# Performance work log

Measured on AMD Instinct MI355X. Metric: run time of the kernel, lower is better.

Reference implementation:

```python
import math
import jax, jax.numpy as jnp
import numpy as np

N, L, D, H = 2, 2048, 1024, 16
DK = D // H  # 64


def setup_inputs() -> dict:
    key = jax.random.key(0)
    k1, k2, k3, k4, k5 = jax.random.split(key, 5)
    scale = 1.0 / math.sqrt(D)
    return {
        "values": jax.random.normal(k1, (N, L, D), dtype=jnp.float32),
        "keys": jax.random.normal(k2, (N, L, D), dtype=jnp.float32),
        "queries": jax.random.normal(k3, (N, L, D), dtype=jnp.float32),
        "fc_out_w": jax.random.normal(k4, (D, D), dtype=jnp.float32) * scale,
        "fc_out_b": jax.random.normal(k5, (D,), dtype=jnp.float32) * scale,
    }


def reference(values, keys, queries, fc_out_w, fc_out_b):
    n, q_len, _ = queries.shape
    k_len = keys.shape[1]
    v = values.reshape(n, k_len, H, DK)
    k = keys.reshape(n, k_len, H, DK)
    q = queries.reshape(n, q_len, H, DK)
    # NOTE: the original module never applies its per-head Linear layers (dead code),
    # and scales logits AFTER the QK einsum.
    energy = jnp.einsum('nqhd,nkhd->nhqk', q, k)  # [N,H,q,k]
    p_attn = jax.nn.softmax(energy / math.sqrt(DK), axis=3)
    attn = jnp.einsum('nhqk,nkhd->nqhd', p_attn, v).reshape(n, q_len, H * DK)
    # fc_out: torch Linear -> x @ W.T + b
    return attn @ fc_out_w.T + fc_out_b
```

## Files before the change

### kernel.cpp

```cpp
#include <hip/hip_runtime.h>
#include <hip/hip_bf16.h>

#define NBATCH 2
#define SEQ    2048
#define DMODEL 1024
#define NHEAD  16
#define DHEAD  64
#define NHTOT  (NBATCH*NHEAD)

typedef __attribute__((ext_vector_type(8))) short          short8;
typedef __attribute__((ext_vector_type(4))) float          f32x4;
typedef __attribute__((ext_vector_type(4))) unsigned short ushort4v;

__device__ __forceinline__ unsigned short f2bf(float x) {
  union { __hip_bfloat16 b; unsigned short u; } c;
  c.b = __float2bfloat16(x);
  return c.u;
}

__device__ __forceinline__ void gl_lds16(const unsigned short* g, unsigned short* l) {
  __builtin_amdgcn_global_load_lds(
      (const __attribute__((address_space(1))) void*)g,
      (__attribute__((address_space(3))) void*)l, 16, 0, 0);
}

__global__ __launch_bounds__(256) void cvt_qk(const float* __restrict__ q,
                                              const float* __restrict__ k,
                                              unsigned short* __restrict__ qb,
                                              unsigned short* __restrict__ kb) {
  const float QSCALE = 0.125f * 1.44269504088896340736f;
  int e = (blockIdx.x * 256 + threadIdx.x) * 4;
  int n = e >> 21;
  int r = e & ((1 << 21) - 1);
  int l = r >> 10;
  int c = r & 1023;
  int h = c >> 6;
  int d = c & 63;
  size_t dst = ((size_t)(n * NHEAD + h) * SEQ + l) * DHEAD + d;
  float4 qv = *reinterpret_cast<const float4*>(q + e);
  float4 kv = *reinterpret_cast<const float4*>(k + e);
  ushort4v qo, ko;
  qo.x = f2bf(qv.x * QSCALE); qo.y = f2bf(qv.y * QSCALE);
  qo.z = f2bf(qv.z * QSCALE); qo.w = f2bf(qv.w * QSCALE);
  ko.x = f2bf(kv.x); ko.y = f2bf(kv.y); ko.z = f2bf(kv.z); ko.w = f2bf(kv.w);
  *reinterpret_cast<ushort4v*>(qb + dst) = qo;
  *reinterpret_cast<ushort4v*>(kb + dst) = ko;
}

__global__ __launch_bounds__(256) void vtrans(const float* __restrict__ v,
                                              unsigned short* __restrict__ vt) {
  __shared__ unsigned short t[64][66];
  int bid = blockIdx.x;
  int nh = bid >> 5;
  int lt = bid & 31;
  int n = nh >> 4, h = nh & 15;
  int lbase = lt * 64;
  #pragma unroll
  for (int j = 0; j < 16; ++j) {
    int e = j * 256 + threadIdx.x;
    int l = e >> 6, d = e & 63;
    float x = v[((size_t)n * SEQ + lbase + l) * DMODEL + h * DHEAD + d];
    t[l][d] = f2bf(x);
  }
  __syncthreads();
  #pragma unroll
  for (int j = 0; j < 16; ++j) {
    int e = j * 256 + threadIdx.x;
    int d = e >> 6, l = e & 63;
    vt[((size_t)nh * DHEAD + d) * SEQ + lbase + l] = t[l][d];
  }
}

__global__ __launch_bounds__(256) void cvt_w(const float* __restrict__ w,
                                             unsigned short* __restrict__ wb) {
  int e = (blockIdx.x * 256 + threadIdx.x) * 4;
  float4 wv = *reinterpret_cast<const float4*>(w + e);
  ushort4v wo;
  wo.x = f2bf(wv.x); wo.y = f2bf(wv.y); wo.z = f2bf(wv.z); wo.w = f2bf(wv.w);
  *reinterpret_cast<ushort4v*>(wb + e) = wo;
}

__global__ __launch_bounds__(256) void attn_fwd(const unsigned short* __restrict__ Qb,
                                                const unsigned short* __restrict__ Kb,
                                                const unsigned short* __restrict__ Vt,
                                                unsigned short* __restrict__ Ab) {
  __shared__ __align__(16) unsigned short kbuf[2][64 * 64];
  __shared__ __align__(16) unsigned short vbuf[2][64 * 64];
  __shared__ __align__(16) unsigned short pbuf[4][16][72];

  const int bid = blockIdx.x;
  const int nh = bid >> 5;
  const int qt = bid & 31;
  const int tid = threadIdx.x;
  const int wave = tid >> 6;
  const int lane = tid & 63;
  const int l15 = lane & 15, l4 = lane >> 4;

  const unsigned short* Kb_nh = Kb + (size_t)nh * SEQ * DHEAD;
  const unsigned short* Vt_nh = Vt + (size_t)nh * DHEAD * SEQ;

  const unsigned short* Qrow =
      Qb + ((size_t)nh * SEQ + qt * 64 + wave * 16 + l15) * DHEAD + l4 * 8;
  short8 bq0 = *reinterpret_cast<const short8*>(Qrow);
  short8 bq1 = *reinterpret_cast<const short8*>(Qrow + 32);

  float m_run = -3.0e38f, l_run = 0.f;
  f32x4 acc[4];
  #pragma unroll
  for (int d = 0; d < 4; ++d) acc[d] = (f32x4){0.f, 0.f, 0.f, 0.f};

  auto stage = [&](int buf, int kk) {
    #pragma unroll
    for (int j = 0; j < 2; ++j) {
      int c = j * 256 + tid;
      int row = c >> 3, cs = c & 7;
      int cg = cs ^ (row & 7);
      int cb = j * 256 + (tid & 192);
      gl_lds16(Kb_nh + (size_t)(kk + row) * DHEAD + cg * 8, &kbuf[buf][cb * 8]);
      gl_lds16(Vt_nh + (size_t)row * SEQ + kk + cg * 8, &vbuf[buf][cb * 8]);
    }
  };

  stage(0, 0);
  __syncthreads();

  const int NT = SEQ / 64;
  for (int it = 0; it < NT; ++it) {
    int cur = it & 1;
    if (it + 1 < NT) stage(cur ^ 1, (it + 1) * 64);

    const unsigned short* kb = kbuf[cur];
    const unsigned short* vb = vbuf[cur];

    f32x4 s[4];
    #pragma unroll
    for (int t = 0; t < 4; ++t) {
      int row = t * 16 + l15;
      int sw = row & 7;
      short8 ak0 = *reinterpret_cast<const short8*>(kb + row * 64 + ((l4 ^ sw) * 8));
      short8 ak1 = *reinterpret_cast<const short8*>(kb + row * 64 + (((l4 + 4) ^ sw) * 8));
      f32x4 z = (f32x4){0.f, 0.f, 0.f, 0.f};
      z = __builtin_amdgcn_mfma_f32_16x16x32_bf16(ak0, bq0, z, 0, 0, 0);
      z = __builtin_amdgcn_mfma_f32_16x16x32_bf16(ak1, bq1, z, 0, 0, 0);
      s[t] = z;
    }

    float mx = s[0][0];
    #pragma unroll
    for (int t = 0; t < 4; ++t)
      #pragma unroll
      for (int r = 0; r < 4; ++r) mx = fmaxf(mx, s[t][r]);
    mx = fmaxf(mx, __shfl_xor(mx, 16));
    mx = fmaxf(mx, __shfl_xor(mx, 32));
    float mnew = fmaxf(m_run, mx);
    float corr = exp2f(m_run - mnew);
    m_run = mnew;
    float sum = 0.f;
    #pragma unroll
    for (int t = 0; t < 4; ++t)
      #pragma unroll
      for (int r = 0; r < 4; ++r) {
        float p = exp2f(s[t][r] - mnew);
        s[t][r] = p;
        sum += p;
      }
    sum += __shfl_xor(sum, 16);
    sum += __shfl_xor(sum, 32);
    l_run = l_run * corr + sum;

    #pragma unroll
    for (int r = 0; r < 4; ++r) {
      float cb_ = __shfl(corr, l4 * 4 + r);
      #pragma unroll
      for (int dd = 0; dd < 4; ++dd) acc[dd][r] *= cb_;
    }

    #pragma unroll
    for (int t = 0; t < 4; ++t) {
      ushort4v pk;
      pk.x = f2bf(s[t][0]); pk.y = f2bf(s[t][1]);
      pk.z = f2bf(s[t][2]); pk.w = f2bf(s[t][3]);
      *reinterpret_cast<ushort4v*>(&pbuf[wave][l15][t * 16 + l4 * 4]) = pk;
    }
    asm volatile("s_waitcnt lgkmcnt(0)" ::: "memory");
    __builtin_amdgcn_sched_barrier(0);
    short8 pa0 = *reinterpret_cast<const short8*>(&pbuf[wave][l15][l4 * 8]);
    short8 pa1 = *reinterpret_cast<const short8*>(&pbuf[wave][l15][32 + l4 * 8]);

    #pragma unroll
    for (int dd = 0; dd < 4; ++dd) {
      int row = dd * 16 + l15;
      int sw = row & 7;
      short8 bv0 = *reinterpret_cast<const short8*>(vb + row * 64 + ((l4 ^ sw) * 8));
      short8 bv1 = *reinterpret_cast<const short8*>(vb + row * 64 + (((l4 + 4) ^ sw) * 8));
      acc[dd] = __builtin_amdgcn_mfma_f32_16x16x32_bf16(pa0, bv0, acc[dd], 0, 0, 0);
      acc[dd] = __builtin_amdgcn_mfma_f32_16x16x32_bf16(pa1, bv1, acc[dd], 0, 0, 0);
    }
    __syncthreads();
  }

  int n = nh >> 4, hd = nh & 15;
  #pragma unroll
  for (int r = 0; r < 4; ++r) {
    float lf = __shfl(l_run, l4 * 4 + r);
    float inv = 1.0f / lf;
    size_t ob = ((size_t)n * SEQ + qt * 64 + wave * 16 + l4 * 4 + r) * DMODEL +
                hd * DHEAD;
    #pragma unroll
    for (int dd = 0; dd < 4; ++dd)
      Ab[ob + dd * 16 + l15] = f2bf(acc[dd][r] * inv);
  }
}

__global__ __launch_bounds__(256) void fc_gemm(const unsigned short* __restrict__ Ab,
                                               const unsigned short* __restrict__ Wb,
                                               const float* __restrict__ bias,
                                               float* __restrict__ out) {
  __shared__ __align__(16) unsigned short At[2][64 * 32];
  __shared__ __align__(16) unsigned short Bt[2][64 * 32];
  const int bid = blockIdx.x;
  const int bm = bid >> 4;
  const int bn = bid & 15;
  const int tid = threadIdx.x;
  const int wave = tid >> 6, lane = tid & 63;
  const int wr = wave >> 1, wc = wave & 1;
  const int l15 = lane & 15, l4 = lane >> 4;

  f32x4 acc[2][2];
  #pragma unroll
  for (int i = 0; i < 2; ++i)
    #pragma unroll
    for (int j = 0; j < 2; ++j) acc[i][j] = (f32x4){0.f, 0.f, 0.f, 0.f};

  auto stage = [&](int buf, int k0) {
    int row = tid >> 2, cs = tid & 3;
    int cb = tid & 192;
    gl_lds16(Ab + (size_t)(bm * 64 + row) * DMODEL + k0 + cs * 8, &At[buf][cb * 8]);
    gl_lds16(Wb + (size_t)(bn * 64 + row) * DMODEL + k0 + cs * 8, &Bt[buf][cb * 8]);
  };

  stage(0, 0);
  __syncthreads();

  const int NT = DMODEL / 32;
  for (int it = 0; it < NT; ++it) {
    int cur = it & 1;
    if (it + 1 < NT) stage(cur ^ 1, (it + 1) * 32);

    short8 a0 = *reinterpret_cast<const short8*>(&At[cur][(wr * 32 + l15) * 32 + l4 * 8]);
    short8 a1 = *reinterpret_cast<const short8*>(&At[cur][(wr * 32 + 16 + l15) * 32 + l4 * 8]);
    short8 b0 = *reinterpret_cast<const short8*>(&Bt[cur][(wc * 32 + l15) * 32 + l4 * 8]);
    short8 b1 = *reinterpret_cast<const short8*>(&Bt[cur][(wc * 32 + 16 + l15) * 32 + l4 * 8]);
    acc[0][0] = __builtin_amdgcn_mfma_f32_16x16x32_bf16(a0, b0, acc[0][0], 0, 0, 0);
    acc[0][1] = __builtin_amdgcn_mfma_f32_16x16x32_bf16(a0, b1, acc[0][1], 0, 0, 0);
    acc[1][0] = __builtin_amdgcn_mfma_f32_16x16x32_bf16(a1, b0, acc[1][0], 0, 0, 0);
    acc[1][1] = __builtin_amdgcn_mfma_f32_16x16x32_bf16(a1, b1, acc[1][1], 0, 0, 0);
    __syncthreads();
  }

  #pragma unroll
  for (int m = 0; m < 2; ++m)
    #pragma unroll
    for (int nn = 0; nn < 2; ++nn) {
      int col = bn * 64 + wc * 32 + nn * 16 + l15;
      float bv = bias[col];
      #pragma unroll
      for (int r = 0; r < 4; ++r) {
        int row = bm * 64 + wr * 32 + m * 16 + l4 * 4 + r;
        out[(size_t)row * DMODEL + col] = acc[m][nn][r] + bv;
      }
    }
}

extern "C" void kernel_launch(void* const* d_in, const int* in_sizes, int n_in,
                              void* d_out, int out_size, void* d_ws, size_t ws_size,
                              hipStream_t stream) {
  const float* values  = (const float*)d_in[0];
  const float* keys    = (const float*)d_in[1];
  const float* queries = (const float*)d_in[2];
  const float* fc_w    = (const float*)d_in[3];
  const float* fc_b    = (const float*)d_in[4];
  float* out = (float*)d_out;

  char* ws = (char*)d_ws;
  const size_t QKV_BYTES = (size_t)NHTOT * SEQ * DHEAD * 2;
  unsigned short* Qb = (unsigned short*)(ws);
  unsigned short* Kb = (unsigned short*)(ws + QKV_BYTES);
  unsigned short* Vt = (unsigned short*)(ws + 2 * QKV_BYTES);
  unsigned short* Wb = (unsigned short*)(ws + 3 * QKV_BYTES);
  unsigned short* Ab = (unsigned short*)(ws + 3 * QKV_BYTES + (size_t)DMODEL * DMODEL * 2);

  cvt_qk<<<4096, 256, 0, stream>>>(queries, keys, Qb, Kb);
  vtrans<<<1024, 256, 0, stream>>>(values, Vt);
  cvt_w<<<1024, 256, 0, stream>>>(fc_w, Wb);
  attn_fwd<<<NHTOT * (SEQ / 64), 256, 0, stream>>>(Qb, Kb, Vt, Ab);
  fc_gemm<<<(NBATCH * SEQ / 64) * (DMODEL / 64), 256, 0, stream>>>(Ab, Wb, fc_b, out);
}
```

Measured before the change: 220.1 us.

## Restructure attention with 32x32 MFMA, register P permute, lazy rescale, and bigger GEMM tiles

```diff
diff --git a/kernel.cpp b/kernel.cpp
--- a/kernel.cpp
+++ b/kernel.cpp
@@ -8,14 +8,21 @@
 #define DHEAD  64
 #define NHTOT  (NBATCH*NHEAD)
 
-typedef __attribute__((ext_vector_type(8))) short          short8;
-typedef __attribute__((ext_vector_type(4))) float          f32x4;
-typedef __attribute__((ext_vector_type(4))) unsigned short ushort4v;
+typedef __attribute__((ext_vector_type(8)))  short          short8;
+typedef __attribute__((ext_vector_type(4)))  float          f32x4;
+typedef __attribute__((ext_vector_type(16))) float          f32x16;
+typedef __attribute__((ext_vector_type(4)))  unsigned short ushort4v;
 
 __device__ __forceinline__ unsigned short f2bf(float x) {
   union { __hip_bfloat16 b; unsigned short u; } c;
   c.b = __float2bfloat16(x);
   return c.u;
+}
+
+__device__ __forceinline__ unsigned int cvt_pk_bf16(float lo, float hi) {
+  unsigned int r;
+  asm("v_cvt_pk_bf16_f32 %0, %1, %2" : "=v"(r) : "v"(lo), "v"(hi));
+  return r;
 }
 
 __device__ __forceinline__ void gl_lds16(const unsigned short* g, unsigned short* l) {
@@ -80,45 +87,49 @@
   *reinterpret_cast<ushort4v*>(wb + e) = wo;
 }
 
-__global__ __launch_bounds__(256) void attn_fwd(const unsigned short* __restrict__ Qb,
-                                                const unsigned short* __restrict__ Kb,
-                                                const unsigned short* __restrict__ Vt,
-                                                unsigned short* __restrict__ Ab) {
+__global__ __launch_bounds__(512, 2) void attn_fwd(const unsigned short* __restrict__ Qb,
+                                                   const unsigned short* __restrict__ Kb,
+                                                   const unsigned short* __restrict__ Vt,
+                                                   unsigned short* __restrict__ Ab) {
   __shared__ __align__(16) unsigned short kbuf[2][64 * 64];
   __shared__ __align__(16) unsigned short vbuf[2][64 * 64];
-  __shared__ __align__(16) unsigned short pbuf[4][16][72];
+  __shared__ __align__(16) unsigned short obuf[4][32][72];
 
   const int bid = blockIdx.x;
-  const int nh = bid >> 5;
-  const int qt = bid & 31;
-  const int tid = threadIdx.x;
+  const int nh = (bid & 7) * 4 + (bid >> 6);
+  const int qt = (bid >> 3) & 7;
+  const int tid  = threadIdx.x;
   const int wave = tid >> 6;
   const int lane = tid & 63;
-  const int l15 = lane & 15, l4 = lane >> 4;
+  const int l31  = lane & 31;
+  const int hi   = lane >> 5;
 
   const unsigned short* Kb_nh = Kb + (size_t)nh * SEQ * DHEAD;
   const unsigned short* Vt_nh = Vt + (size_t)nh * DHEAD * SEQ;
 
-  const unsigned short* Qrow =
-      Qb + ((size_t)nh * SEQ + qt * 64 + wave * 16 + l15) * DHEAD + l4 * 8;
-  short8 bq0 = *reinterpret_cast<const short8*>(Qrow);
-  short8 bq1 = *reinterpret_cast<const short8*>(Qrow + 32);
-
-  float m_run = -3.0e38f, l_run = 0.f;
-  f32x4 acc[4];
-  #pragma unroll
-  for (int d = 0; d < 4; ++d) acc[d] = (f32x4){0.f, 0.f, 0.f, 0.f};
+  const int qglob = qt * 256 + wave * 32 + l31;
+
+  short8 bq[4];
+  {
+    const unsigned short* Qrow = Qb + ((size_t)nh * SEQ + qglob) * DHEAD + hi * 8;
+    #pragma unroll
+    for (int ds = 0; ds < 4; ++ds)
+      bq[ds] = *reinterpret_cast<const short8*>(Qrow + ds * 16);
+  }
+
+  float m_run = -1e30f, l_run = 0.f;
+  f32x16 acc[2];
+  #pragma unroll
+  for (int dt = 0; dt < 2; ++dt)
+    #pragma unroll
+    for (int r = 0; r < 16; ++r) acc[dt][r] = 0.f;
 
   auto stage = [&](int buf, int kk) {
-    #pragma unroll
-    for (int j = 0; j < 2; ++j) {
-      int c = j * 256 + tid;
-      int row = c >> 3, cs = c & 7;
-      int cg = cs ^ (row & 7);
-      int cb = j * 256 + (tid & 192);
-      gl_lds16(Kb_nh + (size_t)(kk + row) * DHEAD + cg * 8, &kbuf[buf][cb * 8]);
-      gl_lds16(Vt_nh + (size_t)row * SEQ + kk + cg * 8, &vbuf[buf][cb * 8]);
-    }
+    int row = tid >> 3, cs = tid & 7;
+    int cg  = cs ^ (row & 7);
+    int cb  = tid & 448;
+    gl_lds16(Kb_nh + (size_t)(kk + row) * DHEAD + cg * 8, &kbuf[buf][cb * 8]);
+    gl_lds16(Vt_nh + (size_t)row * SEQ + kk + cg * 8,     &vbuf[buf][cb * 8]);
   };
 
   stage(0, 0);
@@ -126,89 +137,120 @@
 
   const int NT = SEQ / 64;
   for (int it = 0; it < NT; ++it) {
-    int cur = it & 1;
+    const int cur = it & 1;
     if (it + 1 < NT) stage(cur ^ 1, (it + 1) * 64);
 
     const unsigned short* kb = kbuf[cur];
     const unsigned short* vb = vbuf[cur];
 
-    f32x4 s[4];
-    #pragma unroll
-    for (int t = 0; t < 4; ++t) {
-      int row = t * 16 + l15;
-      int sw = row & 7;
-      short8 ak0 = *reinterpret_cast<const short8*>(kb + row * 64 + ((l4 ^ sw) * 8));
-      short8 ak1 = *reinterpret_cast<const short8*>(kb + row * 64 + (((l4 + 4) ^ sw) * 8));
-      f32x4 z = (f32x4){0.f, 0.f, 0.f, 0.f};
-      z = __builtin_amdgcn_mfma_f32_16x16x32_bf16(ak0, bq0, z, 0, 0, 0);
-      z = __builtin_amdgcn_mfma_f32_16x16x32_bf16(ak1, bq1, z, 0, 0, 0);
-      s[t] = z;
-    }
-
-    float mx = s[0][0];
-    #pragma unroll
-    for (int t = 0; t < 4; ++t)
-      #pragma unroll
-      for (int r = 0; r < 4; ++r) mx = fmaxf(mx, s[t][r]);
-    mx = fmaxf(mx, __shfl_xor(mx, 16));
-    mx = fmaxf(mx, __shfl_xor(mx, 32));
-    float mnew = fmaxf(m_run, mx);
-    float corr = exp2f(m_run - mnew);
-    m_run = mnew;
+    f32x16 s[2];
+    #pragma unroll
+    for (int kt = 0; kt < 2; ++kt) {
+      #pragma unroll
+      for (int r = 0; r < 16; ++r) s[kt][r] = 0.f;
+      const int row = kt * 32 + l31;
+      const int sw  = row & 7;
+      const unsigned short* kr = kb + row * 64;
+      #pragma unroll
+      for (int ds = 0; ds < 4; ++ds) {
+        short8 ak = *reinterpret_cast<const short8*>(kr + (((ds * 2 + hi) ^ sw) * 8));
+        s[kt] = __builtin_amdgcn_mfma_f32_32x32x16_bf16(ak, bq[ds], s[kt], 0, 0, 0);
+      }
+    }
+
+    float pmax = s[0][0];
+    #pragma unroll
+    for (int kt = 0; kt < 2; ++kt)
+      #pragma unroll
+      for (int r = 0; r < 16; ++r) pmax = fmaxf(pmax, s[kt][r]);
+    pmax = fmaxf(pmax, __shfl_xor(pmax, 32));
+
+    if (!__all(pmax - m_run <= 8.0f)) {
+      float mnew = fmaxf(m_run, pmax);
+      float corr = exp2f(m_run - mnew);
+      l_run *= corr;
+      #pragma unroll
+      for (int dt = 0; dt < 2; ++dt)
+        #pragma unroll
+        for (int r = 0; r < 16; ++r) acc[dt][r] *= corr;
+      m_run = mnew;
+    }
+
     float sum = 0.f;
     #pragma unroll
-    for (int t = 0; t < 4; ++t)
-      #pragma unroll
-      for (int r = 0; r < 4; ++r) {
-        float p = exp2f(s[t][r] - mnew);
-        s[t][r] = p;
+    for (int kt = 0; kt < 2; ++kt)
+      #pragma unroll
+      for (int r = 0; r < 16; ++r) {
+        float p = exp2f(s[kt][r] - m_run);
+        s[kt][r] = p;
         sum += p;
       }
-    sum += __shfl_xor(sum, 16);
     sum += __shfl_xor(sum, 32);
-    l_run = l_run * corr + sum;
-
-    #pragma unroll
-    for (int r = 0; r < 4; ++r) {
-      float cb_ = __shfl(corr, l4 * 4 + r);
-      #pragma unroll
-      for (int dd = 0; dd < 4; ++dd) acc[dd][r] *= cb_;
-    }
-
-    #pragma unroll
-    for (int t = 0; t < 4; ++t) {
-      ushort4v pk;
-      pk.x = f2bf(s[t][0]); pk.y = f2bf(s[t][1]);
-      pk.z = f2bf(s[t][2]); pk.w = f2bf(s[t][3]);
-      *reinterpret_cast<ushort4v*>(&pbuf[wave][l15][t * 16 + l4 * 4]) = pk;
-    }
-    asm volatile("s_waitcnt lgkmcnt(0)" ::: "memory");
-    __builtin_amdgcn_sched_barrier(0);
-    short8 pa0 = *reinterpret_cast<const short8*>(&pbuf[wave][l15][l4 * 8]);
-    short8 pa1 = *reinterpret_cast<const short8*>(&pbuf[wave][l15][32 + l4 * 8]);
-
-    #pragma unroll
-    for (int dd = 0; dd < 4; ++dd) {
-      int row = dd * 16 + l15;
-      int sw = row & 7;
-      short8 bv0 = *reinterpret_cast<const short8*>(vb + row * 64 + ((l4 ^ sw) * 8));
-      short8 bv1 = *reinterpret_cast<const short8*>(vb + row * 64 + (((l4 + 4) ^ sw) * 8));
-      acc[dd] = __builtin_amdgcn_mfma_f32_16x16x32_bf16(pa0, bv0, acc[dd], 0, 0, 0);
-      acc[dd] = __builtin_amdgcn_mfma_f32_16x16x32_bf16(pa1, bv1, acc[dd], 0, 0, 0);
+    l_run += sum;
+
+    unsigned int pk[2][8];
+    #pragma unroll
+    for (int kt = 0; kt < 2; ++kt)
+      #pragma unroll
+      for (int i = 0; i < 8; ++i)
+        pk[kt][i] = cvt_pk_bf16(s[kt][2 * i], s[kt][2 * i + 1]);
+
+    unsigned int pa[4][4];
+    #pragma unroll
+    for (int ks = 0; ks < 4; ++ks) {
+      const int t = ks >> 1, b = (ks & 1) * 4;
+      pa[ks][0] = pk[t][b + 0]; pa[ks][2] = pk[t][b + 2];
+      asm("v_permlane32_swap_b32 %0, %1" : "+v"(pa[ks][0]), "+v"(pa[ks][2]));
+      pa[ks][1] = pk[t][b + 1]; pa[ks][3] = pk[t][b + 3];
+      asm("v_permlane32_swap_b32 %0, %1" : "+v"(pa[ks][1]), "+v"(pa[ks][3]));
+    }
+
+    #pragma unroll
+    for (int dt = 0; dt < 2; ++dt) {
+      const int row = dt * 32 + l31;
+      const int sw  = row & 7;
+      const unsigned short* vr = vb + row * 64;
+      #pragma unroll
+      for (int ks = 0; ks < 4; ++ks) {
+        short8 av = *reinterpret_cast<const short8*>(vr + (((ks * 2 + hi) ^ sw) * 8));
+        union { unsigned int u[4]; short8 s8; } pu;
+        pu.u[0] = pa[ks][0]; pu.u[1] = pa[ks][1];
+        pu.u[2] = pa[ks][2]; pu.u[3] = pa[ks][3];
+        acc[dt] = __builtin_amdgcn_mfma_f32_32x32x16_bf16(av, pu.s8, acc[dt], 0, 0, 0);
+      }
     }
     __syncthreads();
   }
 
-  int n = nh >> 4, hd = nh & 15;
-  #pragma unroll
-  for (int r = 0; r < 4; ++r) {
-    float lf = __shfl(l_run, l4 * 4 + r);
-    float inv = 1.0f / lf;
-    size_t ob = ((size_t)n * SEQ + qt * 64 + wave * 16 + l4 * 4 + r) * DMODEL +
-                hd * DHEAD;
-    #pragma unroll
-    for (int dd = 0; dd < 4; ++dd)
-      Ab[ob + dd * 16 + l15] = f2bf(acc[dd][r] * inv);
+  const float inv = 1.0f / l_run;
+  const int n = nh >> 4, h = nh & 15;
+  #pragma unroll
+  for (int pass = 0; pass < 2; ++pass) {
+    if ((wave >> 2) == pass) {
+      const int w = wave & 3;
+      #pragma unroll
+      for (int dt = 0; dt < 2; ++dt)
+        #pragma unroll
+        for (int q4 = 0; q4 < 4; ++q4) {
+          ushort4v pv;
+          pv.x = f2bf(acc[dt][q4 * 4 + 0] * inv);
+          pv.y = f2bf(acc[dt][q4 * 4 + 1] * inv);
+          pv.z = f2bf(acc[dt][q4 * 4 + 2] * inv);
+          pv.w = f2bf(acc[dt][q4 * 4 + 3] * inv);
+          *reinterpret_cast<ushort4v*>(&obuf[w][l31][dt * 32 + q4 * 8 + hi * 4]) = pv;
+        }
+    }
+    __syncthreads();
+    #pragma unroll
+    for (int rep = 0; rep < 2; ++rep) {
+      int idx = rep * 512 + tid;
+      int qi = idx >> 3, ch = idx & 7;
+      int w = qi >> 5, qr = qi & 31;
+      short8 vv = *reinterpret_cast<const short8*>(&obuf[w][qr][ch * 8]);
+      size_t orow = (size_t)n * SEQ + qt * 256 + pass * 128 + qi;
+      *reinterpret_cast<short8*>(Ab + orow * DMODEL + h * 64 + ch * 8) = vv;
+    }
+    __syncthreads();
   }
 }
 
@@ -216,27 +258,32 @@
                                                const unsigned short* __restrict__ Wb,
                                                const float* __restrict__ bias,
                                                float* __restrict__ out) {
-  __shared__ __align__(16) unsigned short At[2][64 * 32];
-  __shared__ __align__(16) unsigned short Bt[2][64 * 32];
+  __shared__ __align__(16) unsigned short At[2][128 * 32];
+  __shared__ __align__(16) unsigned short Bt[2][128 * 32];
   const int bid = blockIdx.x;
-  const int bm = bid >> 4;
-  const int bn = bid & 15;
+  const int bm = bid >> 3;
+  const int bn = bid & 7;
   const int tid = threadIdx.x;
   const int wave = tid >> 6, lane = tid & 63;
   const int wr = wave >> 1, wc = wave & 1;
   const int l15 = lane & 15, l4 = lane >> 4;
 
-  f32x4 acc[2][2];
-  #pragma unroll
-  for (int i = 0; i < 2; ++i)
-    #pragma unroll
-    for (int j = 0; j < 2; ++j) acc[i][j] = (f32x4){0.f, 0.f, 0.f, 0.f};
+  f32x4 acc[4][4];
+  #pragma unroll
+  for (int i = 0; i < 4; ++i)
+    #pragma unroll
+    for (int j = 0; j < 4; ++j) acc[i][j] = (f32x4){0.f, 0.f, 0.f, 0.f};
 
   auto stage = [&](int buf, int k0) {
-    int row = tid >> 2, cs = tid & 3;
-    int cb = tid & 192;
-    gl_lds16(Ab + (size_t)(bm * 64 + row) * DMODEL + k0 + cs * 8, &At[buf][cb * 8]);
-    gl_lds16(Wb + (size_t)(bn * 64 + row) * DMODEL + k0 + cs * 8, &Bt[buf][cb * 8]);
+    #pragma unroll
+    for (int j = 0; j < 2; ++j) {
+      int c = j * 256 + tid;
+      int row = c >> 2, cs = c & 3;
+      int cg = cs ^ (row & 3);
+      int cb = j * 256 + (tid & 192);
+      gl_lds16(Ab + (size_t)(bm * 128 + row) * DMODEL + k0 + cg * 8, &At[buf][cb * 8]);
+      gl_lds16(Wb + (size_t)(bn * 128 + row) * DMODEL + k0 + cg * 8, &Bt[buf][cb * 8]);
+    }
   };
 
   stage(0, 0);
@@ -247,27 +294,35 @@
     int cur = it & 1;
     if (it + 1 < NT) stage(cur ^ 1, (it + 1) * 32);
 
-    short8 a0 = *reinterpret_cast<const short8*>(&At[cur][(wr * 32 + l15) * 32 + l4 * 8]);
-    short8 a1 = *reinterpret_cast<const short8*>(&At[cur][(wr * 32 + 16 + l15) * 32 + l4 * 8]);
-    short8 b0 = *reinterpret_cast<const short8*>(&Bt[cur][(wc * 32 + l15) * 32 + l4 * 8]);
-    short8 b1 = *reinterpret_cast<const short8*>(&Bt[cur][(wc * 32 + 16 + l15) * 32 + l4 * 8]);
-    acc[0][0] = __builtin_amdgcn_mfma_f32_16x16x32_bf16(a0, b0, acc[0][0], 0, 0, 0);
-    acc[0][1] = __builtin_amdgcn_mfma_f32_16x16x32_bf16(a0, b1, acc[0][1], 0, 0, 0);
-    acc[1][0] = __builtin_amdgcn_mfma_f32_16x16x32_bf16(a1, b0, acc[1][0], 0, 0, 0);
-    acc[1][1] = __builtin_amdgcn_mfma_f32_16x16x32_bf16(a1, b1, acc[1][1], 0, 0, 0);
+    short8 af[4], bf[4];
+    #pragma unroll
+    for (int mt = 0; mt < 4; ++mt) {
+      int row = wr * 64 + mt * 16 + l15;
+      af[mt] = *reinterpret_cast<const short8*>(&At[cur][row * 32 + ((l4 ^ (l15 & 3)) * 8)]);
+    }
+    #pragma unroll
+    for (int nt = 0; nt < 4; ++nt) {
+      int row = wc * 64 + nt * 16 + l15;
+      bf[nt] = *reinterpret_cast<const short8*>(&Bt[cur][row * 32 + ((l4 ^ (l15 & 3)) * 8)]);
+    }
+    #pragma unroll
+    for (int mt = 0; mt < 4; ++mt)
+      #pragma unroll
+      for (int nt = 0; nt < 4; ++nt)
+        acc[mt][nt] = __builtin_amdgcn_mfma_f32_16x16x32_bf16(af[mt], bf[nt], acc[mt][nt], 0, 0, 0);
     __syncthreads();
   }
 
   #pragma unroll
-  for (int m = 0; m < 2; ++m)
-    #pragma unroll
-    for (int nn = 0; nn < 2; ++nn) {
-      int col = bn * 64 + wc * 32 + nn * 16 + l15;
+  for (int mt = 0; mt < 4; ++mt)
+    #pragma unroll
+    for (int nt = 0; nt < 4; ++nt) {
+      int col = bn * 128 + wc * 64 + nt * 16 + l15;
       float bv = bias[col];
       #pragma unroll
       for (int r = 0; r < 4; ++r) {
-        int row = bm * 64 + wr * 32 + m * 16 + l4 * 4 + r;
-        out[(size_t)row * DMODEL + col] = acc[m][nn][r] + bv;
+        int row = bm * 128 + wr * 64 + mt * 16 + l4 * 4 + r;
+        out[(size_t)row * DMODEL + col] = acc[mt][nt][r] + bv;
       }
     }
 }
@@ -293,6 +348,6 @@
   cvt_qk<<<4096, 256, 0, stream>>>(queries, keys, Qb, Kb);
   vtrans<<<1024, 256, 0, stream>>>(values, Vt);
   cvt_w<<<1024, 256, 0, stream>>>(fc_w, Wb);
-  attn_fwd<<<NHTOT * (SEQ / 64), 256, 0, stream>>>(Qb, Kb, Vt, Ab);
-  fc_gemm<<<(NBATCH * SEQ / 64) * (DMODEL / 64), 256, 0, stream>>>(Ab, Wb, fc_b, out);
-}
+  attn_fwd<<<NHTOT * (SEQ / 256), 512, 0, stream>>>(Qb, Kb, Vt, Ab);
+  fc_gemm<<<(NBATCH * SEQ / 128) * (DMODEL / 128), 256, 0, stream>>>(Ab, Wb, fc_b, out);
+}
```

Result: faster. 198.3 us (-9.9%).
